# Optimization experiments

Hardware: AMD Instinct MI355X
Metric: run time of the kernel (lower is better)

The kernel has to match this reference:

```python
import jax, jax.numpy as jnp
import numpy as np

B, IN, H, MID = 16384, 256, 512, 64
GRID_SIZE, ORDER = 5, 3
GRID_LO, GRID_HI = -1.0, 1.0
NB = GRID_SIZE + ORDER  # 8 spline basis functions per input feature
LN_EPS = 1e-5


def make_grid(in_features):
    h = (GRID_HI - GRID_LO) / GRID_SIZE
    g = np.arange(-ORDER, GRID_SIZE + ORDER + 1, dtype=np.float32) * h + GRID_LO
    return jnp.asarray(np.tile(g, (in_features, 1)))  # (in, grid_size + 2*order + 1)


def layer_norm(x, g, b):
    mu = jnp.mean(x, axis=-1, keepdims=True)
    var = jnp.var(x, axis=-1, keepdims=True)
    return (x - mu) * jax.lax.rsqrt(var + LN_EPS) * g + b


def b_splines(x, grid):
    # x: (B, in), grid: (in, G). Cox-de Boor recursion (efficient-kan convention).
    xe = x[:, :, None]
    bases = ((xe >= grid[:, :-1]) & (xe < grid[:, 1:])).astype(x.dtype)
    for k in range(1, ORDER + 1):
        left = (xe - grid[:, :-(k + 1)]) / (grid[:, k:-1] - grid[:, :-(k + 1)])
        right = (grid[:, k + 1:] - xe) / (grid[:, k + 1:] - grid[:, 1:-k])
        bases = left * bases[:, :, :-1] + right * bases[:, :, 1:]
    return bases  # (B, in, NB)


def kan_linear(x, base_w, spline_w, scaler, grid):
    # base path: silu(x) @ W_base^T ; spline path: B-spline bases contracted with scaled spline weights
    base = jax.nn.silu(x) @ base_w.T
    bs = b_splines(x, grid)
    spline = jnp.einsum('bik,oik->bo', bs, spline_w * scaler[:, :, None])
    return base + spline


def setup_inputs() -> dict:
    key = jax.random.key(0)
    ks = jax.random.split(key, 24)

    def n(k, shape, fan_in):
        return jax.random.normal(k, shape, dtype=jnp.float32) / np.sqrt(fan_in)

    H2 = 2 * H
    return {
        'x': jax.random.normal(ks[0], (B, IN), jnp.float32),
        'h_prev': jax.random.normal(ks[1], (B, H), jnp.float32),
        'ip_w': n(ks[2], (H, IN), IN), 'ip_b': jnp.zeros((H,), jnp.float32),
        'rg_w': n(ks[3], (H, H2), H2), 'rg_b': jnp.zeros((H,), jnp.float32),
        'rg_g': jnp.ones((H,), jnp.float32), 'rg_beta': jnp.zeros((H,), jnp.float32),
        'ug_w': n(ks[4], (H, H2), H2), 'ug_b': jnp.zeros((H,), jnp.float32),
        'ug_g': jnp.ones((H,), jnp.float32), 'ug_beta': jnp.zeros((H,), jnp.float32),
        'k1_base': n(ks[5], (MID, H2), H2),
        'k1_spline': n(ks[6], (MID, H2, NB), H2) * 0.1,
        'k1_scaler': n(ks[7], (MID, H2), H2) + 1.0,
        'grid1': make_grid(H2),
        'k2_base': n(ks[8], (H, MID), MID),
        'k2_spline': n(ks[9], (H, MID, NB), MID) * 0.1,
        'k2_scaler': n(ks[10], (H, MID), MID) + 1.0,
        'grid2': make_grid(MID),
        'cn_g': jnp.ones((H,), jnp.float32), 'cn_b': jnp.zeros((H,), jnp.float32),
        'rp_w': n(ks[11], (H, H2), H2), 'rp_b': jnp.zeros((H,), jnp.float32),
    }


def reference(x, h_prev, ip_w, ip_b, rg_w, rg_b, rg_g, rg_beta, ug_w, ug_b, ug_g, ug_beta,
              k1_base, k1_spline, k1_scaler, grid1, k2_base, k2_spline, k2_scaler, grid2,
              cn_g, cn_b, rp_w, rp_b):
    x_proj = x @ ip_w.T + ip_b
    combined = jnp.concatenate([x_proj, h_prev], axis=1)  # (B, 2H)
    # reset gate is computed in the original forward but never used; kept for faithfulness
    reset = jnp.tanh(layer_norm(combined @ rg_w.T + rg_b, rg_g, rg_beta))  # noqa: F841
    update = jax.nn.sigmoid(layer_norm(combined @ ug_w.T + ug_b, ug_g, ug_beta))
    # KAN candidate: [2H] -> 64 -> H
    mid = kan_linear(combined, k1_base, k1_spline, k1_scaler, grid1)
    h_cand = kan_linear(mid, k2_base, k2_spline, k2_scaler, grid2)
    residual = combined @ rp_w.T + rp_b
    h_cand = layer_norm(h_cand + residual, cn_g, cn_b)
    h_cand = layer_norm(h_cand, cn_g, cn_b)  # same LayerNorm applied twice, as in source
    h_cand = jax.nn.silu(h_cand)
    h_t = (1.0 - update) * h_prev + update * h_cand
    return h_t
```

## Files before the change

### kernel.cpp

```cpp
#include <hip/hip_runtime.h>
#include <hip/hip_bf16.h>

#define BATCH 16384

typedef __attribute__((ext_vector_type(8))) short short8;
typedef __attribute__((ext_vector_type(4))) float f32x4;

typedef const __attribute__((address_space(1))) uint* gas_t;
typedef __attribute__((address_space(3))) uint* las_t;

__device__ __forceinline__ void gl_lds16(const void* g, void* l) {
    __builtin_amdgcn_global_load_lds((gas_t)g, (las_t)l, 16, 0, 0);
}

__device__ __forceinline__ float bf2f(uint u) { union { uint u; float f; } v; v.u = u << 16; return v.f; }
__device__ __forceinline__ ushort f2bf(float f) {
    union { float f; uint u; } v; v.f = f;
    uint r = v.u + 0x7fffu + ((v.u >> 16) & 1u);
    return (ushort)(r >> 16);
}
__device__ __forceinline__ uint pack2(float a, float b) { return (uint)f2bf(a) | ((uint)f2bf(b) << 16); }
__device__ __forceinline__ uint pack_trunc(float lo, float hi) {
    return __builtin_amdgcn_perm(__float_as_uint(hi), __float_as_uint(lo), 0x07060302u);
}
__device__ __forceinline__ float sigmoidf_(float x) { return __builtin_amdgcn_rcpf(1.0f + __expf(-x)); }
__device__ __forceinline__ float siluf_(float x)    { return x * sigmoidf_(x); }

__device__ __forceinline__ void bases_packed(float x, float g0, float inv_h, uint o[4]) {
    float u = (x - g0) * inv_h;
    float fl = floorf(u);
    float f = u - fl;
    float f2 = f * f, f3 = f2 * f;
    float Ca = f3 * (1.0f / 6.0f);
    float Cb = (1.0f / 6.0f) + 0.5f * (f + f2 - f3);
    float Cc = (2.0f / 3.0f) + 0.5f * f3 - f2;
    float Cd = (1.0f / 6.0f) + 0.5f * (f2 - f) - f3 * (1.0f / 6.0f);
    int t0 = (int)fl;
    t0 = max(-8, min(t0, 19));
    uint dlo = pack_trunc(Cd, Cc);
    uint dhi = pack_trunc(Cb, Ca);
    unsigned long long D = (unsigned long long)dlo | ((unsigned long long)dhi << 32);
    int sp = t0 * 16 - 48;
    unsigned long long l1 = D << (sp & 63);
    unsigned long long r1 = D >> ((-sp) & 63);
    unsigned long long r2 = D >> ((64 - sp) & 63);
    unsigned long long l2 = D << ((sp - 64) & 63);
    unsigned long long lo = (sp >= 0) ? (sp < 64 ? l1 : 0ull) : (sp > -64 ? r1 : 0ull);
    unsigned long long hi = (sp > 0 && sp < 128) ? (sp < 64 ? r2 : l2) : 0ull;
    o[0] = (uint)lo; o[1] = (uint)(lo >> 32); o[2] = (uint)hi; o[3] = (uint)(hi >> 32);
}


__global__ __launch_bounds__(256) void cvt_bf(const float* __restrict__ src, ushort* __restrict__ dst, int n8) {
    int t = blockIdx.x * 256 + threadIdx.x;
    if (t >= n8) return;
    const float4* s = (const float4*)src;
    float4 a = s[t * 2], b = s[t * 2 + 1];
    uint4 o; o.x = pack2(a.x, a.y); o.y = pack2(a.z, a.w); o.z = pack2(b.x, b.y); o.w = pack2(b.z, b.w);
    ((uint4*)dst)[t] = o;
}

__global__ __launch_bounds__(256) void copy_h_bf(const float* __restrict__ hp, ushort* __restrict__ acat) {
    int t = blockIdx.x * 256 + threadIdx.x;
    int b = t >> 6, j = (t & 63) * 8;
    const float4* s = (const float4*)(hp + (size_t)b * 512 + j);
    float4 a = s[0], c = s[1];
    uint4 o; o.x = pack2(a.x, a.y); o.y = pack2(a.z, a.w); o.z = pack2(c.x, c.y); o.w = pack2(c.z, c.w);
    *(uint4*)(acat + (size_t)b * 1600 + 512 + j) = o;
}

__global__ __launch_bounds__(256) void prep_w1aug(const float* __restrict__ k1b, const float* __restrict__ k1s,
                                                  const float* __restrict__ k1sc, ushort* __restrict__ w) {
    int t = blockIdx.x * 256 + threadIdx.x;
    if (t >= 64 * 9216) return;
    int n = t / 9216, r = t % 9216;
    int klog = (r & ~63) | ((((r >> 3) & 7) ^ (n & 7)) << 3) | (r & 7);
    float v;
    if (klog < 1024) v = k1b[n * 1024 + klog];
    else { int i = (klog - 1024) >> 3, k = (klog - 1024) & 7; v = k1s[(n * 1024 + i) * 8 + k] * k1sc[n * 1024 + i]; }
    w[t] = f2bf(v);
}

__global__ __launch_bounds__(256) void prep_wcat(const float* __restrict__ rp, const float* __restrict__ k2b,
                                                 const float* __restrict__ k2s, const float* __restrict__ k2sc,
                                                 ushort* __restrict__ w) {
    int t = blockIdx.x * 256 + threadIdx.x;
    if (t >= 512 * 1600) return;
    int n = t / 1600, c = t % 1600;
    float v;
    if (c < 1024) v = rp[n * 1024 + c];
    else if (c < 1088) v = k2b[n * 64 + (c - 1024)];
    else { int i = (c - 1088) >> 3, k = (c - 1088) & 7; v = k2s[(n * 64 + i) * 8 + k] * k2sc[n * 64 + i]; }
    w[t] = f2bf(v);
}

__global__ __launch_bounds__(256) void gemm_mfma(const ushort* __restrict__ A, int lda,
                                                 const ushort* __restrict__ Wt, int ldw,
                                                 const float* __restrict__ bias,
                                                 ushort* __restrict__ C, int ldc, int K) {
    __shared__ ushort As[2][128 * 64];
    __shared__ ushort Bs[2][128 * 64];
    const int tid = threadIdx.x;
    const int w = tid >> 6, lane = tid & 63;
    const int fr = lane & 15, fq = lane >> 4;
    const int m0 = blockIdx.x * 128, n0 = blockIdx.y * 128;
    const int wm = w & 1, wn = w >> 1;

    const int srow8 = lane >> 3;
    const int scol  = ((lane & 7) ^ srow8) << 3;
    const ushort* gA[4]; const ushort* gB[4]; int fa[4];
#pragma unroll
    for (int j = 0; j < 4; ++j) {
        int rowj = (j * 4 + w) * 8 + srow8;
        fa[j] = (j * 4 + w) * 512 + lane * 8;
        gA[j] = A  + (size_t)(m0 + rowj) * lda + scol;
        gB[j] = Wt + (size_t)(n0 + rowj) * ldw + scol;
    }
    const int nt = K / 64;
#pragma unroll
    for (int j = 0; j < 4; ++j) {
        gl_lds16(gA[j], &As[0][fa[j]]); gl_lds16(gB[j], &Bs[0][fa[j]]);
        gA[j] += 64; gB[j] += 64;
    }
    f32x4 acc[4][4] = {};
    int cur = 0;
    for (int t = 0; t < nt; ++t) {
        __syncthreads();
        if (t + 1 < nt) {
#pragma unroll
            for (int j = 0; j < 4; ++j) {
                gl_lds16(gA[j], &As[cur ^ 1][fa[j]]); gl_lds16(gB[j], &Bs[cur ^ 1][fa[j]]);
                gA[j] += 64; gB[j] += 64;
            }
        }
#pragma unroll
        for (int s = 0; s < 2; ++s) {
            const int csw = ((s * 4 + fq) ^ (fr & 7)) << 3;
            short8 af[4], bv[4];
#pragma unroll
            for (int mi = 0; mi < 4; ++mi)
                af[mi] = *(const short8*)(&As[cur][(wm * 64 + mi * 16 + fr) * 64 + csw]);
#pragma unroll
            for (int ni = 0; ni < 4; ++ni)
                bv[ni] = *(const short8*)(&Bs[cur][(wn * 64 + ni * 16 + fr) * 64 + csw]);
#pragma unroll
            for (int mi = 0; mi < 4; ++mi)
#pragma unroll
                for (int ni = 0; ni < 4; ++ni)
                    acc[mi][ni] = __builtin_amdgcn_mfma_f32_16x16x32_bf16(af[mi], bv[ni], acc[mi][ni], 0, 0, 0);
        }
        cur ^= 1;
    }
#pragma unroll
    for (int mi = 0; mi < 4; ++mi) {
#pragma unroll
        for (int ni = 0; ni < 4; ++ni) {
            int n = n0 + wn * 64 + ni * 16 + fr;
            float bvs = bias[n];
#pragma unroll
            for (int r = 0; r < 4; ++r) {
                int m = m0 + wm * 64 + mi * 16 + fq * 4 + r;
                C[(size_t)m * ldc + n] = f2bf(acc[mi][ni][r] + bvs);
            }
        }
    }
}

__global__ __launch_bounds__(256) void kan1_mfma(const ushort* __restrict__ acat,
                                                 const ushort* __restrict__ w1aug,
                                                 const float* __restrict__ grid1,
                                                 float* __restrict__ midp) {
    __shared__ ushort As[32 * 64];
    __shared__ ushort Bs[64 * 64];
    const int tid = threadIdx.x;
    const int w = tid >> 6, lane = tid & 63;
    const int fr = lane & 15, fq = lane >> 4;
    const int m0 = blockIdx.x * 32;
    const int kb = blockIdx.y;
    const int kstart = kb * 2304;
    const float g0 = grid1[0];
    const float inv_h = 1.0f / (grid1[1] - g0);

    const int srow = tid >> 3, sc = tid & 7;
    ushort* aWr = As + srow * 64 + ((sc ^ (srow & 7)) << 3);
    const ushort* combRow = acat + (size_t)(m0 + srow) * 1600;

    const int bn = tid >> 3, bpc = tid & 7;
    const ushort* gB0 = w1aug + (size_t)bn * 9216 + kstart + bpc * 8;
    const ushort* gB1 = w1aug + (size_t)(bn + 32) * 9216 + kstart + bpc * 8;
    ushort* lB0 = Bs + tid * 8;
    ushort* lB1 = Bs + 2048 + tid * 8;

    const int wm = w & 1, wn = w >> 1;
    const int arow = wm * 16 + fr;
    const ushort* aRd = As + arow * 64;
    const int axor = arow & 7;

    f32x4 acc[2] = {};
    for (int step = 0; step < 36; ++step) {
        const int k0 = kstart + step * 64;
        gl_lds16(gB0, lB0); gl_lds16(gB1, lB1);
        gB0 += 64; gB1 += 64;
        uint o[4];
        if (k0 < 1024) {
            uint4 raw = *(const uint4*)(combRow + k0 + sc * 8);
            uint rr[4] = {raw.x, raw.y, raw.z, raw.w};
#pragma unroll
            for (int p = 0; p < 4; ++p) {
                float loF = siluf_(bf2f(rr[p] & 0xffffu));
                float hiF = siluf_(bf2f(rr[p] >> 16));
                o[p] = pack_trunc(loF, hiF);
            }
        } else {
            int i = ((k0 - 1024) >> 3) + sc;
            float x = bf2f((uint)combRow[i]);
            bases_packed(x, g0, inv_h, o);
        }
        uint4 o4; o4.x = o[0]; o4.y = o[1]; o4.z = o[2]; o4.w = o[3];
        *(uint4*)aWr = o4;
        __syncthreads();
#pragma unroll
        for (int s = 0; s < 2; ++s) {
            short8 af = *(const short8*)(aRd + (((s * 4 + fq) ^ axor) << 3));
#pragma unroll
            for (int ni = 0; ni < 2; ++ni) {
                int n = wn * 32 + ni * 16 + fr;
                short8 bv = *(const short8*)(Bs + n * 64 + (((s * 4 + fq) ^ (n & 7)) << 3));
                acc[ni] = __builtin_amdgcn_mfma_f32_16x16x32_bf16(af, bv, acc[ni], 0, 0, 0);
            }
        }
        __syncthreads();
    }
    float* outp = midp + (size_t)kb * (BATCH * 64);
#pragma unroll
    for (int ni = 0; ni < 2; ++ni)
#pragma unroll
        for (int r = 0; r < 4; ++r)
            outp[(size_t)(m0 + wm * 16 + fq * 4 + r) * 64 + wn * 32 + ni * 16 + fr] = acc[ni][r];
}

__global__ __launch_bounds__(256) void bs2_kernel(const float* __restrict__ midp,
                                                  const float* __restrict__ grid2,
                                                  ushort* __restrict__ acat) {
    int t = blockIdx.x * 256 + threadIdx.x;
    if (t >= BATCH * 64) return;
    float x = midp[t] + midp[BATCH * 64 + t] + midp[2 * BATCH * 64 + t] + midp[3 * BATCH * 64 + t];
    int b = t >> 6, i = t & 63;
    float g0 = grid2[0], inv_h = 1.0f / (grid2[1] - g0);
    acat[(size_t)b * 1600 + 1024 + i] = f2bf(siluf_(x));
    uint o[4];
    bases_packed(x, g0, inv_h, o);
    uint4 o4; o4.x = o[0]; o4.y = o[1]; o4.z = o[2]; o4.w = o[3];
    *(uint4*)&acat[(size_t)b * 1600 + 1088 + i * 8] = o4;
}

__device__ __forceinline__ void block_reduce_2(float& a, float& b, float (*red)[4]) {
#pragma unroll
    for (int off = 32; off; off >>= 1) {
        a += __shfl_xor(a, off, 64);
        b += __shfl_xor(b, off, 64);
    }
    int lane = threadIdx.x & 63, wid = threadIdx.x >> 6;
    if (lane == 0) { red[0][wid] = a; red[1][wid] = b; }
    __syncthreads();
    a = red[0][0] + red[0][1] + red[0][2] + red[0][3];
    b = red[1][0] + red[1][1] + red[1][2] + red[1][3];
}

__global__ __launch_bounds__(256) void final2(const ushort* __restrict__ ug,
                                              const ushort* __restrict__ hcb,
                                              const float* __restrict__ hprev,
                                              const float* __restrict__ ug_g,
                                              const float* __restrict__ ug_beta,
                                              const float* __restrict__ cg,
                                              const float* __restrict__ cb,
                                              float* __restrict__ out) {
    int row = blockIdx.x, tid = threadIdx.x;
    __shared__ float rA[2][4], rB[2][4], rC[2][4];
    float u0 = bf2f((uint)ug[(size_t)row * 512 + tid]);
    float u1 = bf2f((uint)ug[(size_t)row * 512 + tid + 256]);
    float h0 = bf2f((uint)hcb[(size_t)row * 512 + tid]);
    float h1 = bf2f((uint)hcb[(size_t)row * 512 + tid + 256]);
    float s = u0 + u1, ss = u0 * u0 + u1 * u1;
    block_reduce_2(s, ss, rA);
    float mu = s * (1.0f / 512.0f);
    float var = ss * (1.0f / 512.0f) - mu * mu;
    float r = rsqrtf(var + 1e-5f);
    float uu0 = sigmoidf_((u0 - mu) * r * ug_g[tid] + ug_beta[tid]);
    float uu1 = sigmoidf_((u1 - mu) * r * ug_g[tid + 256] + ug_beta[tid + 256]);
    float cg0 = cg[tid], cg1 = cg[tid + 256], cb0 = cb[tid], cb1 = cb[tid + 256];
    float s2 = h0 + h1, ss2 = h0 * h0 + h1 * h1;
    block_reduce_2(s2, ss2, rB);
    float mu2 = s2 * (1.0f / 512.0f);
    float var2 = ss2 * (1.0f / 512.0f) - mu2 * mu2;
    float r2 = rsqrtf(var2 + 1e-5f);
    float w0 = (h0 - mu2) * r2 * cg0 + cb0;
    float w1 = (h1 - mu2) * r2 * cg1 + cb1;
    float s3 = w0 + w1, ss3 = w0 * w0 + w1 * w1;
    block_reduce_2(s3, ss3, rC);
    float mu3 = s3 * (1.0f / 512.0f);
    float var3 = ss3 * (1.0f / 512.0f) - mu3 * mu3;
    float r3 = rsqrtf(var3 + 1e-5f);
    float c0 = siluf_((w0 - mu3) * r3 * cg0 + cb0);
    float c1 = siluf_((w1 - mu3) * r3 * cg1 + cb1);
    size_t o0 = (size_t)row * 512 + tid, o1 = o0 + 256;
    float hp0 = hprev[o0], hp1 = hprev[o1];
    out[o0] = (1.0f - uu0) * hp0 + uu0 * c0;
    out[o1] = (1.0f - uu1) * hp1 + uu1 * c1;
}

extern "C" void kernel_launch(void* const* d_in, const int* in_sizes, int n_in,
                              void* d_out, int out_size, void* d_ws, size_t ws_size,
                              hipStream_t stream) {
    const float* x        = (const float*)d_in[0];
    const float* h_prev   = (const float*)d_in[1];
    const float* ip_w     = (const float*)d_in[2];
    const float* ip_b     = (const float*)d_in[3];
    const float* ug_w     = (const float*)d_in[8];
    const float* ug_b     = (const float*)d_in[9];
    const float* ug_g     = (const float*)d_in[10];
    const float* ug_beta  = (const float*)d_in[11];
    const float* k1_base  = (const float*)d_in[12];
    const float* k1_spline= (const float*)d_in[13];
    const float* k1_scaler= (const float*)d_in[14];
    const float* grid1    = (const float*)d_in[15];
    const float* k2_base  = (const float*)d_in[16];
    const float* k2_spline= (const float*)d_in[17];
    const float* k2_scaler= (const float*)d_in[18];
    const float* grid2    = (const float*)d_in[19];
    const float* cn_g     = (const float*)d_in[20];
    const float* cn_b     = (const float*)d_in[21];
    const float* rp_w     = (const float*)d_in[22];
    const float* rp_b     = (const float*)d_in[23];
    float* out = (float*)d_out;
    char* W = (char*)d_ws;

    ushort* Acat   = (ushort*)(W);
    ushort* ug_bf  = (ushort*)(W + 52428800);
    ushort* hc_bf  = (ushort*)(W + 69206016);
    float*  midp   = (float*) (W + 85983232);
    ushort* x_bf   = (ushort*)(W + 102760448);
    ushort* ipw_bf = (ushort*)(W + 111149056);
    ushort* ugw_bf = (ushort*)(W + 111411200);
    ushort* wcat   = (ushort*)(W + 112459776);
    ushort* w1aug  = (ushort*)(W + 114098176);

    hipLaunchKernelGGL(cvt_bf, dim3(2048), dim3(256), 0, stream, x, x_bf, BATCH * 256 / 8);
    hipLaunchKernelGGL(cvt_bf, dim3(64),   dim3(256), 0, stream, ip_w, ipw_bf, 512 * 256 / 8);
    hipLaunchKernelGGL(cvt_bf, dim3(256),  dim3(256), 0, stream, ug_w, ugw_bf, 512 * 1024 / 8);
    hipLaunchKernelGGL(prep_wcat, dim3(3200), dim3(256), 0, stream, rp_w, k2_base, k2_spline, k2_scaler, wcat);
    hipLaunchKernelGGL(prep_w1aug, dim3(2304), dim3(256), 0, stream, k1_base, k1_spline, k1_scaler, w1aug);
    hipLaunchKernelGGL(copy_h_bf, dim3(4096), dim3(256), 0, stream, h_prev, Acat);

    hipLaunchKernelGGL(gemm_mfma, dim3(BATCH / 128, 4), dim3(256), 0, stream,
                       x_bf, 256, ipw_bf, 256, ip_b, Acat, 1600, 256);

    hipLaunchKernelGGL(gemm_mfma, dim3(BATCH / 128, 4), dim3(256), 0, stream,
                       Acat, 1600, ugw_bf, 1024, ug_b, ug_bf, 512, 1024);

    hipLaunchKernelGGL(kan1_mfma, dim3(BATCH / 32, 4), dim3(256), 0, stream, Acat, w1aug, grid1, midp);
    hipLaunchKernelGGL(bs2_kernel, dim3(BATCH * 64 / 256), dim3(256), 0, stream, midp, grid2, Acat);

    hipLaunchKernelGGL(gemm_mfma, dim3(BATCH / 128, 4), dim3(256), 0, stream,
                       Acat, 1600, wcat, 1600, rp_b, hc_bf, 512, 1600);

    hipLaunchKernelGGL(final2, dim3(BATCH), dim3(256), 0, stream, ug_bf, hc_bf, h_prev, ug_g, ug_beta, cn_g, cn_b, out);
}
```

Before: 173.4 us.

## Fuse weight prep, fold x conversion into ip GEMM, restructure KAN1 split-K

The four weight-prep kernels become one launch, and the separate x-to-bf16 pass is removed: gemm_ip converts fp32 x into LDS on the fly. gemm_ip and copy_h_sil also write a precomputed SiLU(combined) bf16 buffer, so kan1 streams its base-path A tiles directly with global-to-LDS loads instead of applying SiLU per step. kan1 moves to 64-row tiles with double-buffered LDS and an 8-way split-K, and bs2 reduces eight partials instead of four. This trades extra workspace and more partial-sum traffic for fewer launches, less redundant SiLU work and better overlap of loads with MFMA.

```diff
diff --git a/kernel.cpp b/kernel.cpp
--- a/kernel.cpp
+++ b/kernel.cpp
@@ -50,48 +50,45 @@
     o[0] = (uint)lo; o[1] = (uint)(lo >> 32); o[2] = (uint)hi; o[3] = (uint)(hi >> 32);
 }
 
-
-__global__ __launch_bounds__(256) void cvt_bf(const float* __restrict__ src, ushort* __restrict__ dst, int n8) {
+__global__ __launch_bounds__(256) void prep_all(const float* __restrict__ ip_w, const float* __restrict__ ug_w,
+                                                const float* __restrict__ rp,  const float* __restrict__ k2b,
+                                                const float* __restrict__ k2s, const float* __restrict__ k2sc,
+                                                const float* __restrict__ k1b, const float* __restrict__ k1s,
+                                                const float* __restrict__ k1sc,
+                                                ushort* __restrict__ ipw, ushort* __restrict__ ugw,
+                                                ushort* __restrict__ wcat, ushort* __restrict__ w1aug) {
     int t = blockIdx.x * 256 + threadIdx.x;
-    if (t >= n8) return;
-    const float4* s = (const float4*)src;
-    float4 a = s[t * 2], b = s[t * 2 + 1];
-    uint4 o; o.x = pack2(a.x, a.y); o.y = pack2(a.z, a.w); o.z = pack2(b.x, b.y); o.w = pack2(b.z, b.w);
-    ((uint4*)dst)[t] = o;
-}
-
-__global__ __launch_bounds__(256) void copy_h_bf(const float* __restrict__ hp, ushort* __restrict__ acat) {
+    if (t < 131072) { ipw[t] = f2bf(ip_w[t]); return; }
+    t -= 131072;
+    if (t < 524288) { ugw[t] = f2bf(ug_w[t]); return; }
+    t -= 524288;
+    if (t < 819200) {
+        int n = t / 1600, c = t % 1600; float v;
+        if (c < 1024) v = rp[n * 1024 + c];
+        else if (c < 1088) v = k2b[n * 64 + (c - 1024)];
+        else { int i = (c - 1088) >> 3, k = (c - 1088) & 7; v = k2s[(n * 64 + i) * 8 + k] * k2sc[n * 64 + i]; }
+        wcat[t] = f2bf(v); return;
+    }
+    t -= 819200;
+    if (t < 589824) {
+        int n = t / 9216, c = t % 9216; float v;
+        if (c < 1024) v = k1b[n * 1024 + c];
+        else { int i = (c - 1024) >> 3, k = (c - 1024) & 7; v = k1s[(n * 1024 + i) * 8 + k] * k1sc[n * 1024 + i]; }
+        w1aug[t] = f2bf(v);
+    }
+}
+
+__global__ __launch_bounds__(256) void copy_h_sil(const float* __restrict__ hp,
+                                                  ushort* __restrict__ acat, ushort* __restrict__ ssw) {
     int t = blockIdx.x * 256 + threadIdx.x;
     int b = t >> 6, j = (t & 63) * 8;
     const float4* s = (const float4*)(hp + (size_t)b * 512 + j);
     float4 a = s[0], c = s[1];
     uint4 o; o.x = pack2(a.x, a.y); o.y = pack2(a.z, a.w); o.z = pack2(c.x, c.y); o.w = pack2(c.z, c.w);
     *(uint4*)(acat + (size_t)b * 1600 + 512 + j) = o;
-}
-
-__global__ __launch_bounds__(256) void prep_w1aug(const float* __restrict__ k1b, const float* __restrict__ k1s,
-                                                  const float* __restrict__ k1sc, ushort* __restrict__ w) {
-    int t = blockIdx.x * 256 + threadIdx.x;
-    if (t >= 64 * 9216) return;
-    int n = t / 9216, r = t % 9216;
-    int klog = (r & ~63) | ((((r >> 3) & 7) ^ (n & 7)) << 3) | (r & 7);
-    float v;
-    if (klog < 1024) v = k1b[n * 1024 + klog];
-    else { int i = (klog - 1024) >> 3, k = (klog - 1024) & 7; v = k1s[(n * 1024 + i) * 8 + k] * k1sc[n * 1024 + i]; }
-    w[t] = f2bf(v);
-}
-
-__global__ __launch_bounds__(256) void prep_wcat(const float* __restrict__ rp, const float* __restrict__ k2b,
-                                                 const float* __restrict__ k2s, const float* __restrict__ k2sc,
-                                                 ushort* __restrict__ w) {
-    int t = blockIdx.x * 256 + threadIdx.x;
-    if (t >= 512 * 1600) return;
-    int n = t / 1600, c = t % 1600;
-    float v;
-    if (c < 1024) v = rp[n * 1024 + c];
-    else if (c < 1088) v = k2b[n * 64 + (c - 1024)];
-    else { int i = (c - 1088) >> 3, k = (c - 1088) & 7; v = k2s[(n * 64 + i) * 8 + k] * k2sc[n * 64 + i]; }
-    w[t] = f2bf(v);
+    uint4 q; q.x = pack2(siluf_(a.x), siluf_(a.y)); q.y = pack2(siluf_(a.z), siluf_(a.w));
+    q.z = pack2(siluf_(c.x), siluf_(c.y)); q.w = pack2(siluf_(c.z), siluf_(c.w));
+    *(uint4*)(ssw + (size_t)b * 1024 + 512 + j) = q;
 }
 
 __global__ __launch_bounds__(256) void gemm_mfma(const ushort* __restrict__ A, int lda,
@@ -166,77 +163,185 @@
     }
 }
 
+__global__ __launch_bounds__(256) void gemm_ip(const float* __restrict__ X,
+                                               const ushort* __restrict__ Wt,
+                                               const float* __restrict__ bias,
+                                               ushort* __restrict__ acat,
+                                               ushort* __restrict__ ssw) {
+    __shared__ ushort As[2][128 * 64];
+    __shared__ ushort Bs[2][128 * 64];
+    const int tid = threadIdx.x;
+    const int w = tid >> 6, lane = tid & 63;
+    const int fr = lane & 15, fq = lane >> 4;
+    const int m0 = blockIdx.x * 128, n0 = blockIdx.y * 128;
+    const int wm = w & 1, wn = w >> 1;
+
+    const int srow8 = lane >> 3;
+    const int scol = ((lane & 7) ^ srow8) << 3;
+    const ushort* gB[4]; int fa[4];
+#pragma unroll
+    for (int j = 0; j < 4; ++j) {
+        int rowj = (j * 4 + w) * 8 + srow8;
+        fa[j] = (j * 4 + w) * 512 + lane * 8;
+        gB[j] = Wt + (size_t)(n0 + rowj) * 256 + scol;
+    }
+    const float* gA[4]; int ar[4];
+#pragma unroll
+    for (int j = 0; j < 4; ++j) {
+        int rj = j * 32 + (tid >> 3);
+        int lc = (tid & 7) ^ (rj & 7);
+        ar[j] = rj * 64 + (tid & 7) * 8;
+        gA[j] = X + (size_t)(m0 + rj) * 256 + lc * 8;
+    }
+    float4 va[4], vb[4];
+#pragma unroll
+    for (int j = 0; j < 4; ++j) { gl_lds16(gB[j], &Bs[0][fa[j]]); gB[j] += 64; }
+#pragma unroll
+    for (int j = 0; j < 4; ++j) { va[j] = *(const float4*)gA[j]; vb[j] = *(const float4*)(gA[j] + 4); gA[j] += 64; }
+#pragma unroll
+    for (int j = 0; j < 4; ++j) {
+        uint4 o; o.x = pack2(va[j].x, va[j].y); o.y = pack2(va[j].z, va[j].w);
+        o.z = pack2(vb[j].x, vb[j].y); o.w = pack2(vb[j].z, vb[j].w);
+        *(uint4*)&As[0][ar[j]] = o;
+    }
+    f32x4 acc[4][4] = {};
+    int cur = 0;
+    for (int t = 0; t < 4; ++t) {
+        __syncthreads();
+        if (t < 3) {
+#pragma unroll
+            for (int j = 0; j < 4; ++j) { gl_lds16(gB[j], &Bs[cur ^ 1][fa[j]]); gB[j] += 64; }
+#pragma unroll
+            for (int j = 0; j < 4; ++j) { va[j] = *(const float4*)gA[j]; vb[j] = *(const float4*)(gA[j] + 4); gA[j] += 64; }
+        }
+#pragma unroll
+        for (int s = 0; s < 2; ++s) {
+            const int csw = ((s * 4 + fq) ^ (fr & 7)) << 3;
+            short8 af[4], bv[4];
+#pragma unroll
+            for (int mi = 0; mi < 4; ++mi)
+                af[mi] = *(const short8*)(&As[cur][(wm * 64 + mi * 16 + fr) * 64 + csw]);
+#pragma unroll
+            for (int ni = 0; ni < 4; ++ni)
+                bv[ni] = *(const short8*)(&Bs[cur][(wn * 64 + ni * 16 + fr) * 64 + csw]);
+#pragma unroll
+            for (int mi = 0; mi < 4; ++mi)
+#pragma unroll
+                for (int ni = 0; ni < 4; ++ni)
+                    acc[mi][ni] = __builtin_amdgcn_mfma_f32_16x16x32_bf16(af[mi], bv[ni], acc[mi][ni], 0, 0, 0);
+        }
+        if (t < 3) {
+#pragma unroll
+            for (int j = 0; j < 4; ++j) {
+                uint4 o; o.x = pack2(va[j].x, va[j].y); o.y = pack2(va[j].z, va[j].w);
+                o.z = pack2(vb[j].x, vb[j].y); o.w = pack2(vb[j].z, vb[j].w);
+                *(uint4*)&As[cur ^ 1][ar[j]] = o;
+            }
+        }
+        cur ^= 1;
+    }
+#pragma unroll
+    for (int mi = 0; mi < 4; ++mi) {
+#pragma unroll
+        for (int ni = 0; ni < 4; ++ni) {
+            int n = n0 + wn * 64 + ni * 16 + fr;
+            float bvs = bias[n];
+#pragma unroll
+            for (int r = 0; r < 4; ++r) {
+                int m = m0 + wm * 64 + mi * 16 + fq * 4 + r;
+                float val = acc[mi][ni][r] + bvs;
+                acat[(size_t)m * 1600 + n] = f2bf(val);
+                ssw[(size_t)m * 1024 + n] = f2bf(siluf_(val));
+            }
+        }
+    }
+}
+
 __global__ __launch_bounds__(256) void kan1_mfma(const ushort* __restrict__ acat,
+                                                 const ushort* __restrict__ ssw,
                                                  const ushort* __restrict__ w1aug,
                                                  const float* __restrict__ grid1,
                                                  float* __restrict__ midp) {
-    __shared__ ushort As[32 * 64];
-    __shared__ ushort Bs[64 * 64];
+    __shared__ ushort As[2][64 * 64];
+    __shared__ ushort Bs[2][64 * 64];
     const int tid = threadIdx.x;
     const int w = tid >> 6, lane = tid & 63;
     const int fr = lane & 15, fq = lane >> 4;
-    const int m0 = blockIdx.x * 32;
+    const int m0 = blockIdx.x * 64;
     const int kb = blockIdx.y;
-    const int kstart = kb * 2304;
     const float g0 = grid1[0];
     const float inv_h = 1.0f / (grid1[1] - g0);
 
     const int srow = tid >> 3, sc = tid & 7;
-    ushort* aWr = As + srow * 64 + ((sc ^ (srow & 7)) << 3);
-    const ushort* combRow = acat + (size_t)(m0 + srow) * 1600;
-
-    const int bn = tid >> 3, bpc = tid & 7;
-    const ushort* gB0 = w1aug + (size_t)bn * 9216 + kstart + bpc * 8;
-    const ushort* gB1 = w1aug + (size_t)(bn + 32) * 9216 + kstart + bpc * 8;
-    ushort* lB0 = Bs + tid * 8;
-    ushort* lB1 = Bs + 2048 + tid * 8;
-
+    const int xr = srow & 7;
+    const int lc8 = (sc ^ xr) << 3;
+    const ushort* swA0 = ssw + (size_t)(m0 + srow) * 1024 + lc8;
+    const ushort* swA1 = ssw + (size_t)(m0 + srow + 32) * 1024 + lc8;
+    const ushort* wB0  = w1aug + (size_t)srow * 9216 + lc8;
+    const ushort* wB1  = w1aug + (size_t)(srow + 32) * 9216 + lc8;
+    const ushort* aRow0 = acat + (size_t)(m0 + srow) * 1600;
+    const ushort* aRow1 = acat + (size_t)(m0 + srow + 32) * 1600;
+    const int wpo = srow * 64 + lc8;
     const int wm = w & 1, wn = w >> 1;
-    const int arow = wm * 16 + fr;
-    const ushort* aRd = As + arow * 64;
-    const int axor = arow & 7;
-
-    f32x4 acc[2] = {};
-    for (int step = 0; step < 36; ++step) {
-        const int k0 = kstart + step * 64;
-        gl_lds16(gB0, lB0); gl_lds16(gB1, lB1);
-        gB0 += 64; gB1 += 64;
-        uint o[4];
-        if (k0 < 1024) {
-            uint4 raw = *(const uint4*)(combRow + k0 + sc * 8);
-            uint rr[4] = {raw.x, raw.y, raw.z, raw.w};
-#pragma unroll
-            for (int p = 0; p < 4; ++p) {
-                float loF = siluf_(bf2f(rr[p] & 0xffffu));
-                float hiF = siluf_(bf2f(rr[p] >> 16));
-                o[p] = pack_trunc(loF, hiF);
-            }
-        } else {
-            int i = ((k0 - 1024) >> 3) + sc;
-            float x = bf2f((uint)combRow[i]);
-            bases_packed(x, g0, inv_h, o);
-        }
-        uint4 o4; o4.x = o[0]; o4.y = o[1]; o4.z = o[2]; o4.w = o[3];
-        *(uint4*)aWr = o4;
+
+    f32x4 acc[2][2] = {};
+    {
+        int c = kb * 128;
+        gl_lds16(wB0 + c, &Bs[0][tid * 8]); gl_lds16(wB1 + c, &Bs[0][2048 + tid * 8]);
+        gl_lds16(swA0 + c, &As[0][tid * 8]); gl_lds16(swA1 + c, &As[0][2048 + tid * 8]);
+    }
+    int cur = 0;
+    for (int s = 0; s < 18; ++s) {
         __syncthreads();
-#pragma unroll
-        for (int s = 0; s < 2; ++s) {
-            short8 af = *(const short8*)(aRd + (((s * 4 + fq) ^ axor) << 3));
+        if (s + 1 < 18) {
+            int c = (s + 1 < 2) ? kb * 128 + (s + 1) * 64 : 1024 + kb * 1024 + (s - 1) * 64;
+            gl_lds16(wB0 + c, &Bs[cur ^ 1][tid * 8]);
+            gl_lds16(wB1 + c, &Bs[cur ^ 1][2048 + tid * 8]);
+            if (s + 1 < 2) {
+                gl_lds16(swA0 + c, &As[cur ^ 1][tid * 8]);
+                gl_lds16(swA1 + c, &As[cur ^ 1][2048 + tid * 8]);
+            } else {
+                int i = ((c - 1024) >> 3) + sc;
+                float x0 = bf2f((uint)aRow0[i]);
+                float x1 = bf2f((uint)aRow1[i]);
+                uint o0[4], o1[4];
+                bases_packed(x0, g0, inv_h, o0);
+                bases_packed(x1, g0, inv_h, o1);
+                uint4 q0; q0.x = o0[0]; q0.y = o0[1]; q0.z = o0[2]; q0.w = o0[3];
+                uint4 q1; q1.x = o1[0]; q1.y = o1[1]; q1.z = o1[2]; q1.w = o1[3];
+                *(uint4*)&As[cur ^ 1][wpo] = q0;
+                *(uint4*)&As[cur ^ 1][2048 + wpo] = q1;
+            }
+        }
+#pragma unroll
+        for (int s2 = 0; s2 < 2; ++s2) {
+            short8 af[2], bv[2];
+#pragma unroll
+            for (int mi = 0; mi < 2; ++mi) {
+                int arow = wm * 32 + mi * 16 + fr;
+                af[mi] = *(const short8*)(&As[cur][arow * 64 + (((s2 * 4 + fq) ^ (arow & 7)) << 3)]);
+            }
 #pragma unroll
             for (int ni = 0; ni < 2; ++ni) {
-                int n = wn * 32 + ni * 16 + fr;
-                short8 bv = *(const short8*)(Bs + n * 64 + (((s * 4 + fq) ^ (n & 7)) << 3));
-                acc[ni] = __builtin_amdgcn_mfma_f32_16x16x32_bf16(af, bv, acc[ni], 0, 0, 0);
-            }
-        }
-        __syncthreads();
+                int brow = wn * 32 + ni * 16 + fr;
+                bv[ni] = *(const short8*)(&Bs[cur][brow * 64 + (((s2 * 4 + fq) ^ (brow & 7)) << 3)]);
+            }
+#pragma unroll
+            for (int mi = 0; mi < 2; ++mi)
+#pragma unroll
+                for (int ni = 0; ni < 2; ++ni)
+                    acc[mi][ni] = __builtin_amdgcn_mfma_f32_16x16x32_bf16(af[mi], bv[ni], acc[mi][ni], 0, 0, 0);
+        }
+        cur ^= 1;
     }
     float* outp = midp + (size_t)kb * (BATCH * 64);
 #pragma unroll
-    for (int ni = 0; ni < 2; ++ni)
-#pragma unroll
-        for (int r = 0; r < 4; ++r)
-            outp[(size_t)(m0 + wm * 16 + fq * 4 + r) * 64 + wn * 32 + ni * 16 + fr] = acc[ni][r];
+    for (int mi = 0; mi < 2; ++mi)
+#pragma unroll
+        for (int ni = 0; ni < 2; ++ni)
+#pragma unroll
+            for (int r = 0; r < 4; ++r)
+                outp[(size_t)(m0 + wm * 32 + mi * 16 + fq * 4 + r) * 64 + wn * 32 + ni * 16 + fr] = acc[mi][ni][r];
 }
 
 __global__ __launch_bounds__(256) void bs2_kernel(const float* __restrict__ midp,
@@ -244,7 +349,9 @@
                                                   ushort* __restrict__ acat) {
     int t = blockIdx.x * 256 + threadIdx.x;
     if (t >= BATCH * 64) return;
-    float x = midp[t] + midp[BATCH * 64 + t] + midp[2 * BATCH * 64 + t] + midp[3 * BATCH * 64 + t];
+    float x = 0.0f;
+#pragma unroll
+    for (int p = 0; p < 8; ++p) x += midp[(size_t)p * (BATCH * 64) + t];
     int b = t >> 6, i = t & 63;
     float g0 = grid2[0], inv_h = 1.0f / (grid2[1] - g0);
     acat[(size_t)b * 1600 + 1024 + i] = f2bf(siluf_(x));
@@ -335,30 +442,29 @@
     float* out = (float*)d_out;
     char* W = (char*)d_ws;
 
-    ushort* Acat   = (ushort*)(W);
-    ushort* ug_bf  = (ushort*)(W + 52428800);
-    ushort* hc_bf  = (ushort*)(W + 69206016);
-    float*  midp   = (float*) (W + 85983232);
-    ushort* x_bf   = (ushort*)(W + 102760448);
-    ushort* ipw_bf = (ushort*)(W + 111149056);
-    ushort* ugw_bf = (ushort*)(W + 111411200);
-    ushort* wcat   = (ushort*)(W + 112459776);
-    ushort* w1aug  = (ushort*)(W + 114098176);
-
-    hipLaunchKernelGGL(cvt_bf, dim3(2048), dim3(256), 0, stream, x, x_bf, BATCH * 256 / 8);
-    hipLaunchKernelGGL(cvt_bf, dim3(64),   dim3(256), 0, stream, ip_w, ipw_bf, 512 * 256 / 8);
-    hipLaunchKernelGGL(cvt_bf, dim3(256),  dim3(256), 0, stream, ug_w, ugw_bf, 512 * 1024 / 8);
-    hipLaunchKernelGGL(prep_wcat, dim3(3200), dim3(256), 0, stream, rp_w, k2_base, k2_spline, k2_scaler, wcat);
-    hipLaunchKernelGGL(prep_w1aug, dim3(2304), dim3(256), 0, stream, k1_base, k1_spline, k1_scaler, w1aug);
-    hipLaunchKernelGGL(copy_h_bf, dim3(4096), dim3(256), 0, stream, h_prev, Acat);
-
-    hipLaunchKernelGGL(gemm_mfma, dim3(BATCH / 128, 4), dim3(256), 0, stream,
-                       x_bf, 256, ipw_bf, 256, ip_b, Acat, 1600, 256);
+    ushort* Acat    = (ushort*)(W);
+    ushort* ug_bf   = (ushort*)(W + 52428800);
+    ushort* silu_sw = (ushort*)(W + 69206016);
+    float*  midp    = (float*) (W + 102760448);
+    ushort* hc_bf   = (ushort*)(W + 102760448);
+    ushort* ipw_bf  = (ushort*)(W + 136314880);
+    ushort* ugw_bf  = (ushort*)(W + 136577024);
+    ushort* wcat    = (ushort*)(W + 137625600);
+    ushort* w1aug   = (ushort*)(W + 139264000);
+
+    hipLaunchKernelGGL(prep_all, dim3(8064), dim3(256), 0, stream,
+                       ip_w, ug_w, rp_w, k2_base, k2_spline, k2_scaler,
+                       k1_base, k1_spline, k1_scaler, ipw_bf, ugw_bf, wcat, w1aug);
+    hipLaunchKernelGGL(copy_h_sil, dim3(4096), dim3(256), 0, stream, h_prev, Acat, silu_sw);
+
+    hipLaunchKernelGGL(gemm_ip, dim3(BATCH / 128, 4), dim3(256), 0, stream,
+                       x, ipw_bf, ip_b, Acat, silu_sw);
 
     hipLaunchKernelGGL(gemm_mfma, dim3(BATCH / 128, 4), dim3(256), 0, stream,
                        Acat, 1600, ugw_bf, 1024, ug_b, ug_bf, 512, 1024);
 
-    hipLaunchKernelGGL(kan1_mfma, dim3(BATCH / 32, 4), dim3(256), 0, stream, Acat, w1aug, grid1, midp);
+    hipLaunchKernelGGL(kan1_mfma, dim3(BATCH / 64, 8), dim3(256), 0, stream,
+                       Acat, silu_sw, w1aug, grid1, midp);
     hipLaunchKernelGGL(bs2_kernel, dim3(BATCH * 64 / 256), dim3(256), 0, stream, midp, grid2, Acat);
 
     hipLaunchKernelGGL(gemm_mfma, dim3(BATCH / 128, 4), dim3(256), 0, stream,
```

New measurement: 175.2 us. Within noise of the previous version (+1.0%).
